# Performance work log

Hardware: AMD Instinct MI355X
Metric: run time of the kernel (lower is better)

Reference implementation:

```python
import jax, jax.numpy as jnp
import numpy as np

N_WORDS = 64
N_CONT_LABELS = 64
N_DISC_LABELS = 32


def _tuple_indices(n):
    # Enumerate (i, k, l, j) with i <= k, l >= k + 2, l <= j < n, matching the
    # nested Python loops in the original forward. Count is static given n.
    ii, kk, ll, jj = np.indices((n, n, n, n), dtype=np.int16)
    mask = (kk >= ii) & (ll >= kk + 2) & (jj >= ll)
    i = ii[mask].astype(np.int32)
    k = kk[mask].astype(np.int32)
    l = ll[mask].astype(np.int32)
    j = jj[mask].astype(np.int32)
    cont_idx = i * n + j                  # row of flattened disc table
    disc_idx = (k + 1) * n + (l - 1)      # row of flattened gap table
    return cont_idx, disc_idx


def setup_inputs() -> dict:
    key = jax.random.key(0)
    n, Lc, Ld = N_WORDS, N_CONT_LABELS, N_DISC_LABELS
    k0, k1, k2, k3, k4 = jax.random.split(key, 5)
    cont_weights = jax.random.normal(k0, (n, n, Lc), dtype=jnp.float32)
    disc_weights = jax.random.normal(k1, (n, n, Ld), dtype=jnp.float32)
    gap_weights = jax.random.normal(k2, (n, n, Ld), dtype=jnp.float32)
    cont_idx_np, disc_idx_np = _tuple_indices(n)  # T = 677040 for n=64
    T = cont_idx_np.shape[0]
    cont_gold = jax.random.randint(k3, (n, n), 0, Lc + 1, dtype=jnp.int32)
    disc_gold = jax.random.randint(k4, (T,), 0, Ld + 1, dtype=jnp.int32)
    return {
        "cont_weights": cont_weights,
        "disc_weights": disc_weights,
        "gap_weights": gap_weights,
        "cont_gold": cont_gold,
        "disc_gold": disc_gold,
        "cont_idx": jnp.asarray(cont_idx_np),
        "disc_idx": jnp.asarray(disc_idx_np),
    }


def reference(cont_weights, disc_weights, gap_weights, cont_gold, disc_gold,
              cont_idx, disc_idx):
    n = cont_weights.shape[0]
    Lc = cont_weights.shape[2]
    Ld = disc_weights.shape[2]
    dt = cont_weights.dtype
    null = jnp.zeros((n, n, 1), dtype=dt)

    # Continuous constituents: per-cell cross-entropy, masked to upper triangle.
    cw = jnp.concatenate([cont_weights, null], axis=-1)          # [n, n, Lc+1]
    log_z = jax.nn.logsumexp(cw, axis=-1)                        # [n, n]
    gold = jnp.take_along_axis(cw, cont_gold[..., None].astype(jnp.int32),
                               axis=-1)[..., 0]                  # [n, n]
    triu = jnp.triu(jnp.ones((n, n), dtype=dt))
    cont_loss = jnp.sum((log_z - gold) * triu)

    # Discontinuous constituents: gather rows of the two tables, add, CE-sum.
    dw = jnp.concatenate([disc_weights, null], axis=-1).reshape(-1, Ld + 1)
    gw = jnp.concatenate([gap_weights, null], axis=-1).reshape(-1, Ld + 1)
    w = dw[cont_idx] + gw[disc_idx]                              # [T, Ld+1]
    gold_d = jnp.take_along_axis(w, disc_gold[:, None].astype(jnp.int32),
                                 axis=1)[:, 0]                   # [T]
    disc_loss = jnp.sum(jax.nn.logsumexp(w, axis=-1) - gold_d)

    return cont_loss + disc_loss
```

## Files before the change

### kernel.cpp

```cpp
#include <hip/hip_runtime.h>

#define N 64
#define LC 64
#define LD 32
#define NCONT (N * N)
#define CONT_BLOCKS 16
#define NPAIRS 1953

typedef __attribute__((ext_vector_type(8))) short short8;
typedef __attribute__((ext_vector_type(4))) float f32x4;

__device__ inline unsigned f2bf(float f) {
    unsigned u = __float_as_uint(f);
    u += 0x7FFF + ((u >> 16) & 1);
    return u >> 16;
}
__device__ inline float bf2f(unsigned u) {
    return __uint_as_float(u << 16);
}

__device__ inline float block_sum(float v, float* ws) {
    #pragma unroll
    for (int off = 32; off > 0; off >>= 1)
        v += __shfl_down(v, off, 64);
    const int lane = threadIdx.x & 63;
    const int wid  = threadIdx.x >> 6;
    if (lane == 0) ws[wid] = v;
    __syncthreads();
    return ws[0] + ws[1] + ws[2] + ws[3];
}

__global__ __launch_bounds__(256, 8) void loss_kernel(
    const float* __restrict__ cont_w,
    const float* __restrict__ disc_w,
    const float* __restrict__ gap_w,
    const int*   __restrict__ cont_gold,
    const int*   __restrict__ disc_gold,
    float* __restrict__ partials, int T)
{
    __shared__ unsigned short EgB[64 * 32];
    __shared__ unsigned short EdB[64 * 32];
    __shared__ float ws[4];

    float acc = 0.0f;

    if (blockIdx.x < CONT_BLOCKS) {
        const int idx = blockIdx.x * 256 + threadIdx.x;
        const int i = idx >> 6, j = idx & 63;
        if (i <= j) {
            const float4* p = reinterpret_cast<const float4*>(cont_w + idx * LC);
            const int g = cont_gold[idx];
            const float goldv = (g < LC) ? cont_w[idx * LC + g] : 0.0f;
            float s0 = 1.0f, s1 = 0.0f, s2 = 0.0f, s3 = 0.0f;
            #pragma unroll
            for (int q = 0; q < LC / 4; ++q) {
                float4 x = p[q];
                s0 += __expf(x.x); s1 += __expf(x.y);
                s2 += __expf(x.z); s3 += __expf(x.w);
            }
            acc = __logf((s0 + s1) + (s2 + s3)) - goldv;
        }
    } else {
        const int w = blockIdx.x - CONT_BLOCKS;
        int k = (int)((sqrtf(8.0f * (float)w + 1.0f) - 1.0f) * 0.5f);
        while (k * (k + 1) / 2 > w) --k;
        while ((k + 1) * (k + 2) / 2 <= w) ++k;
        const int i = w - k * (k + 1) / 2;
        const int M = 62 - k;

        const int MT   = (M + 15) >> 4;
        const int MT16 = MT << 4;
        const float4* srcD = reinterpret_cast<const float4*>(
            disc_w + ((i << 6) + (k + 2)) * LD);
        const float4* srcG = reinterpret_cast<const float4*>(
            gap_w + (((k + 1) << 6) + (k + 1)) * LD);
        for (int e = threadIdx.x; e < MT16 * 8; e += 256) {
            const int r = e >> 3, ch = e & 7;
            uint2* pd = reinterpret_cast<uint2*>(&EdB[r * 32 + ch * 4]);
            uint2* pg = reinterpret_cast<uint2*>(&EgB[r * 32 + ch * 4]);
            if (r < M) {
                float4 x = srcD[e];
                float4 y = srcG[e];
                uint2 xd = { (f2bf(__expf(x.y)) << 16) | f2bf(__expf(x.x)),
                             (f2bf(__expf(x.w)) << 16) | f2bf(__expf(x.z)) };
                uint2 yg = { (f2bf(__expf(y.y)) << 16) | f2bf(__expf(y.x)),
                             (f2bf(__expf(y.w)) << 16) | f2bf(__expf(y.z)) };
                *pd = xd;
                *pg = yg;
            } else {
                uint2 z = {0u, 0u};
                *pd = z;
                *pg = z;
            }
        }
        __syncthreads();

        const int ntiles = MT * (MT + 1) / 2;
        const int wid  = threadIdx.x >> 6;
        const int lane = threadIdx.x & 63;
        const int r16  = lane & 15;
        const int g4   = lane >> 4;
        for (int p = wid; p < ntiles; p += 4) {
            int tr = 0, base = 0;
            while (base + (MT - tr) <= p) { base += MT - tr; ++tr; }
            const int tc = tr + (p - base);
            short8 a = *reinterpret_cast<const short8*>(
                &EgB[(tr * 16 + r16) * 32 + g4 * 8]);
            short8 b = *reinterpret_cast<const short8*>(
                &EdB[(tc * 16 + r16) * 32 + g4 * 8]);
            f32x4 c = {0.0f, 0.0f, 0.0f, 0.0f};
            c = __builtin_amdgcn_mfma_f32_16x16x32_bf16(a, b, c, 0, 0, 0);
            #pragma unroll
            for (int q = 0; q < 4; ++q) {
                const int l = tr * 16 + g4 * 4 + q;
                const int j = tc * 16 + r16;
                if (j < M && l <= j)
                    acc += __logf(c[q] + 1.0f);
            }
        }

        const int A  = 62 - i;
        const int fA = A * (A + 1) * (A + 2) * (A + 3) / 24;
        const int hA = A * (A + 1) * (A + 2) / 6;
        const int hK = M * (M + 1) * (M + 2) / 6;
        const int t0 = (677040 - fA) + (hA - hK);
        const int cells = M * (M + 1) / 2;

        const int Bc = (cells + 255) >> 8;
        const int c0 = threadIdx.x * Bc;
        const int c1 = min(c0 + Bc, cells);
        if (c0 < c1) {
            const float twoM1 = (float)(2 * M + 1);
            int l = (int)((twoM1 - sqrtf(twoM1 * twoM1 - 8.0f * (float)c0)) * 0.5f);
            if (l < 0) l = 0;
            if (l > M - 1) l = M - 1;
            while (l * M - l * (l - 1) / 2 > c0) --l;
            while ((l + 1) * M - (l + 1) * l / 2 <= c0) ++l;
            int j = l + (c0 - (l * M - l * (l - 1) / 2));
            for (int c = c0; c < c1; ++c) {
                const int g = disc_gold[t0 + c];
                if (g < LD) {
                    const float ed = bf2f(EdB[j * 32 + g]);
                    const float eg = bf2f(EgB[l * 32 + g]);
                    acc -= __logf(ed * eg);
                }
                ++j;
                if (j >= M) { ++l; j = l; }
            }
        }
    }

    const float bsum = block_sum(acc, ws);
    if (threadIdx.x == 0)
        partials[blockIdx.x] = bsum;
}

__global__ __launch_bounds__(1024) void reduce_kernel(
    const float* __restrict__ partials, float* __restrict__ out, int nblocks)
{
    float acc = 0.0f;
    for (int i = threadIdx.x; i < nblocks; i += 1024)
        acc += partials[i];
    #pragma unroll
    for (int off = 32; off > 0; off >>= 1)
        acc += __shfl_down(acc, off, 64);

    __shared__ float ws[16];
    const int lane = threadIdx.x & 63;
    const int wid  = threadIdx.x >> 6;
    if (lane == 0) ws[wid] = acc;
    __syncthreads();
    if (threadIdx.x == 0) {
        float s = 0.0f;
        #pragma unroll
        for (int w = 0; w < 16; ++w) s += ws[w];
        out[0] = s;
    }
}

extern "C" void kernel_launch(void* const* d_in, const int* in_sizes, int n_in,
                              void* d_out, int out_size, void* d_ws, size_t ws_size,
                              hipStream_t stream) {
    const float* cont_w    = (const float*)d_in[0];
    const float* disc_w    = (const float*)d_in[1];
    const float* gap_w     = (const float*)d_in[2];
    const int*   cont_gold = (const int*)d_in[3];
    const int*   disc_gold = (const int*)d_in[4];
    float* out      = (float*)d_out;
    float* partials = (float*)d_ws;
    const int T = in_sizes[4];

    const int blocks = CONT_BLOCKS + NPAIRS;
    loss_kernel<<<blocks, 256, 0, stream>>>(cont_w, disc_w, gap_w, cont_gold,
                                            disc_gold, partials, T);
    reduce_kernel<<<1, 1024, 0, stream>>>(partials, out, blocks);
}
```

Before: 14.04 us.

## Pack four work units per 1024-thread block, drop reduce kernel via atomicAdd

Restructures the launch into 256 blocks of 1024 threads, where each block runs four independent 256-thread teams with their own LDS tiles, each team covering two work units in a fixed two-pass loop. The separate reduction kernel is replaced by a memset and a per-block atomicAdd into the output. This is meant to cut the second kernel launch and the block-scheduling overhead of about two thousand small blocks. In exchange, teams now synchronise block-wide, so the slowest team in a block sets the pace. The LDS writes also go from packed 64-bit stores to scalar 16-bit stores, and the atomic summation order is no longer deterministic.

```diff
diff --git a/kernel.cpp b/kernel.cpp
--- a/kernel.cpp
+++ b/kernel.cpp
@@ -3,8 +3,7 @@
 #define N 64
 #define LC 64
 #define LD 32
-#define NCONT (N * N)
-#define CONT_BLOCKS 16
+#define NUNITS 1969
 #define NPAIRS 1953
 
 typedef __attribute__((ext_vector_type(8))) short short8;
@@ -19,162 +18,155 @@
     return __uint_as_float(u << 16);
 }
 
-__device__ inline float block_sum(float v, float* ws) {
-    #pragma unroll
-    for (int off = 32; off > 0; off >>= 1)
-        v += __shfl_down(v, off, 64);
-    const int lane = threadIdx.x & 63;
-    const int wid  = threadIdx.x >> 6;
-    if (lane == 0) ws[wid] = v;
-    __syncthreads();
-    return ws[0] + ws[1] + ws[2] + ws[3];
-}
-
-__global__ __launch_bounds__(256, 8) void loss_kernel(
+__global__ __launch_bounds__(1024, 4) void loss_kernel(
     const float* __restrict__ cont_w,
     const float* __restrict__ disc_w,
     const float* __restrict__ gap_w,
     const int*   __restrict__ cont_gold,
     const int*   __restrict__ disc_gold,
-    float* __restrict__ partials, int T)
+    float* __restrict__ out)
 {
-    __shared__ unsigned short EgB[64 * 32];
-    __shared__ unsigned short EdB[64 * 32];
-    __shared__ float ws[4];
+    __shared__ unsigned short EgB[4][64 * 32];
+    __shared__ unsigned short EdB[4][64 * 32];
+    __shared__ float ws[16];
+
+    const int team  = threadIdx.x >> 8;
+    const int tid   = threadIdx.x & 255;
+    const int gteam = (int)blockIdx.x * 4 + team;
 
     float acc = 0.0f;
 
-    if (blockIdx.x < CONT_BLOCKS) {
-        const int idx = blockIdx.x * 256 + threadIdx.x;
-        const int i = idx >> 6, j = idx & 63;
-        if (i <= j) {
-            const float4* p = reinterpret_cast<const float4*>(cont_w + idx * LC);
-            const int g = cont_gold[idx];
-            const float goldv = (g < LC) ? cont_w[idx * LC + g] : 0.0f;
-            float s0 = 1.0f, s1 = 0.0f, s2 = 0.0f, s3 = 0.0f;
-            #pragma unroll
-            for (int q = 0; q < LC / 4; ++q) {
-                float4 x = p[q];
-                s0 += __expf(x.x); s1 += __expf(x.y);
-                s2 += __expf(x.z); s3 += __expf(x.w);
-            }
-            acc = __logf((s0 + s1) + (s2 + s3)) - goldv;
-        }
-    } else {
-        const int w = blockIdx.x - CONT_BLOCKS;
-        int k = (int)((sqrtf(8.0f * (float)w + 1.0f) - 1.0f) * 0.5f);
-        while (k * (k + 1) / 2 > w) --k;
-        while ((k + 1) * (k + 2) / 2 <= w) ++k;
-        const int i = w - k * (k + 1) / 2;
-        const int M = 62 - k;
+    #pragma unroll
+    for (int rep = 0; rep < 2; ++rep) {
+        const int u = gteam + rep * 1024;
+        const bool valid   = (u < NUNITS);
+        const bool is_cont = valid && (u < 16);
+        const bool is_pair = valid && (u >= 16);
 
-        const int MT   = (M + 15) >> 4;
-        const int MT16 = MT << 4;
-        const float4* srcD = reinterpret_cast<const float4*>(
-            disc_w + ((i << 6) + (k + 2)) * LD);
-        const float4* srcG = reinterpret_cast<const float4*>(
-            gap_w + (((k + 1) << 6) + (k + 1)) * LD);
-        for (int e = threadIdx.x; e < MT16 * 8; e += 256) {
-            const int r = e >> 3, ch = e & 7;
-            uint2* pd = reinterpret_cast<uint2*>(&EdB[r * 32 + ch * 4]);
-            uint2* pg = reinterpret_cast<uint2*>(&EgB[r * 32 + ch * 4]);
-            if (r < M) {
-                float4 x = srcD[e];
-                float4 y = srcG[e];
-                uint2 xd = { (f2bf(__expf(x.y)) << 16) | f2bf(__expf(x.x)),
-                             (f2bf(__expf(x.w)) << 16) | f2bf(__expf(x.z)) };
-                uint2 yg = { (f2bf(__expf(y.y)) << 16) | f2bf(__expf(y.x)),
-                             (f2bf(__expf(y.w)) << 16) | f2bf(__expf(y.z)) };
-                *pd = xd;
-                *pg = yg;
-            } else {
-                uint2 z = {0u, 0u};
-                *pd = z;
-                *pg = z;
+        int i = 0, k = 0, M = 0, MT = 0;
+        if (is_pair) {
+            const int w = u - 16;
+            k = (int)((sqrtf(8.0f * (float)w + 1.0f) - 1.0f) * 0.5f);
+            while (k * (k + 1) / 2 > w) --k;
+            while ((k + 1) * (k + 2) / 2 <= w) ++k;
+            i = w - k * (k + 1) / 2;
+            M = 62 - k;
+            MT = (M + 15) >> 4;
+
+            const int MT16 = MT << 4;
+            const float4* srcD = reinterpret_cast<const float4*>(
+                disc_w + ((i << 6) + (k + 2)) * LD);
+            const float4* srcG = reinterpret_cast<const float4*>(
+                gap_w + (((k + 1) << 6) + (k + 1)) * LD);
+            for (int e = tid; e < MT16 * 8; e += 256) {
+                const int r = e >> 3, ch = e & 7;
+                unsigned short* pd = &EdB[team][r * 32 + ch * 4];
+                unsigned short* pg = &EgB[team][r * 32 + ch * 4];
+                if (r < M) {
+                    float4 x = srcD[e];
+                    float4 y = srcG[e];
+                    pd[0] = (unsigned short)f2bf(__expf(x.x));
+                    pd[1] = (unsigned short)f2bf(__expf(x.y));
+                    pd[2] = (unsigned short)f2bf(__expf(x.z));
+                    pd[3] = (unsigned short)f2bf(__expf(x.w));
+                    pg[0] = (unsigned short)f2bf(__expf(y.x));
+                    pg[1] = (unsigned short)f2bf(__expf(y.y));
+                    pg[2] = (unsigned short)f2bf(__expf(y.z));
+                    pg[3] = (unsigned short)f2bf(__expf(y.w));
+                } else {
+                    pd[0] = 0; pd[1] = 0; pd[2] = 0; pd[3] = 0;
+                    pg[0] = 0; pg[1] = 0; pg[2] = 0; pg[3] = 0;
+                }
             }
         }
         __syncthreads();
 
-        const int ntiles = MT * (MT + 1) / 2;
-        const int wid  = threadIdx.x >> 6;
-        const int lane = threadIdx.x & 63;
-        const int r16  = lane & 15;
-        const int g4   = lane >> 4;
-        for (int p = wid; p < ntiles; p += 4) {
-            int tr = 0, base = 0;
-            while (base + (MT - tr) <= p) { base += MT - tr; ++tr; }
-            const int tc = tr + (p - base);
-            short8 a = *reinterpret_cast<const short8*>(
-                &EgB[(tr * 16 + r16) * 32 + g4 * 8]);
-            short8 b = *reinterpret_cast<const short8*>(
-                &EdB[(tc * 16 + r16) * 32 + g4 * 8]);
-            f32x4 c = {0.0f, 0.0f, 0.0f, 0.0f};
-            c = __builtin_amdgcn_mfma_f32_16x16x32_bf16(a, b, c, 0, 0, 0);
-            #pragma unroll
-            for (int q = 0; q < 4; ++q) {
-                const int l = tr * 16 + g4 * 4 + q;
-                const int j = tc * 16 + r16;
-                if (j < M && l <= j)
-                    acc += __logf(c[q] + 1.0f);
+        if (is_cont) {
+            const int idx = u * 256 + tid;
+            const int ii = idx >> 6, jj = idx & 63;
+            if (ii <= jj) {
+                const float4* p =
+                    reinterpret_cast<const float4*>(cont_w + idx * LC);
+                const int g = cont_gold[idx];
+                const float goldv = (g < LC) ? cont_w[idx * LC + g] : 0.0f;
+                float s0 = 1.0f, s1 = 0.0f, s2 = 0.0f, s3 = 0.0f;
+                #pragma unroll
+                for (int q = 0; q < LC / 4; ++q) {
+                    float4 x = p[q];
+                    s0 += __expf(x.x); s1 += __expf(x.y);
+                    s2 += __expf(x.z); s3 += __expf(x.w);
+                }
+                acc = __logf((s0 + s1) + (s2 + s3)) - goldv;
+            }
+        } else if (is_pair) {
+            const int ntiles = MT * (MT + 1) / 2;
+            const int wid  = tid >> 6;
+            const int lane = tid & 63;
+            const int r16  = lane & 15;
+            const int g4   = lane >> 4;
+            for (int p = wid; p < ntiles; p += 4) {
+                int tr = 0, base = 0;
+                while (base + (MT - tr) <= p) { base += MT - tr; ++tr; }
+                const int tc = tr + (p - base);
+                short8 a = *reinterpret_cast<const short8*>(
+                    &EgB[team][(tr * 16 + r16) * 32 + g4 * 8]);
+                short8 b = *reinterpret_cast<const short8*>(
+                    &EdB[team][(tc * 16 + r16) * 32 + g4 * 8]);
+                f32x4 c = {0.0f, 0.0f, 0.0f, 0.0f};
+                c = __builtin_amdgcn_mfma_f32_16x16x32_bf16(a, b, c, 0, 0, 0);
+                #pragma unroll
+                for (int q = 0; q < 4; ++q) {
+                    const int l = tr * 16 + g4 * 4 + q;
+                    const int j = tc * 16 + r16;
+                    if (j < M && l <= j)
+                        acc += __logf(c[q] + 1.0f);
+                }
+            }
+
+            const int A  = 62 - i;
+            const int fA = A * (A + 1) * (A + 2) * (A + 3) / 24;
+            const int hA = A * (A + 1) * (A + 2) / 6;
+            const int hK = M * (M + 1) * (M + 2) / 6;
+            const int t0 = (677040 - fA) + (hA - hK);
+            const int cells = M * (M + 1) / 2;
+
+            const int Bc = (cells + 255) >> 8;
+            const int c0 = tid * Bc;
+            const int c1 = min(c0 + Bc, cells);
+            if (c0 < c1) {
+                const float twoM1 = (float)(2 * M + 1);
+                int l = (int)((twoM1 -
+                    sqrtf(twoM1 * twoM1 - 8.0f * (float)c0)) * 0.5f);
+                if (l < 0) l = 0;
+                if (l > M - 1) l = M - 1;
+                while (l * M - l * (l - 1) / 2 > c0) --l;
+                while ((l + 1) * M - (l + 1) * l / 2 <= c0) ++l;
+                int j = l + (c0 - (l * M - l * (l - 1) / 2));
+                for (int c = c0; c < c1; ++c) {
+                    const int g = disc_gold[t0 + c];
+                    if (g < LD) {
+                        const float ed = bf2f(EdB[team][j * 32 + g]);
+                        const float eg = bf2f(EgB[team][l * 32 + g]);
+                        acc -= __logf(ed * eg);
+                    }
+                    ++j;
+                    if (j >= M) { ++l; j = l; }
+                }
             }
         }
-
-        const int A  = 62 - i;
-        const int fA = A * (A + 1) * (A + 2) * (A + 3) / 24;
-        const int hA = A * (A + 1) * (A + 2) / 6;
-        const int hK = M * (M + 1) * (M + 2) / 6;
-        const int t0 = (677040 - fA) + (hA - hK);
-        const int cells = M * (M + 1) / 2;
-
-        const int Bc = (cells + 255) >> 8;
-        const int c0 = threadIdx.x * Bc;
-        const int c1 = min(c0 + Bc, cells);
-        if (c0 < c1) {
-            const float twoM1 = (float)(2 * M + 1);
-            int l = (int)((twoM1 - sqrtf(twoM1 * twoM1 - 8.0f * (float)c0)) * 0.5f);
-            if (l < 0) l = 0;
-            if (l > M - 1) l = M - 1;
-            while (l * M - l * (l - 1) / 2 > c0) --l;
-            while ((l + 1) * M - (l + 1) * l / 2 <= c0) ++l;
-            int j = l + (c0 - (l * M - l * (l - 1) / 2));
-            for (int c = c0; c < c1; ++c) {
-                const int g = disc_gold[t0 + c];
-                if (g < LD) {
-                    const float ed = bf2f(EdB[j * 32 + g]);
-                    const float eg = bf2f(EgB[l * 32 + g]);
-                    acc -= __logf(ed * eg);
-                }
-                ++j;
-                if (j >= M) { ++l; j = l; }
-            }
-        }
+        __syncthreads();
     }
 
-    const float bsum = block_sum(acc, ws);
-    if (threadIdx.x == 0)
-        partials[blockIdx.x] = bsum;
-}
-
-__global__ __launch_bounds__(1024) void reduce_kernel(
-    const float* __restrict__ partials, float* __restrict__ out, int nblocks)
-{
-    float acc = 0.0f;
-    for (int i = threadIdx.x; i < nblocks; i += 1024)
-        acc += partials[i];
     #pragma unroll
     for (int off = 32; off > 0; off >>= 1)
         acc += __shfl_down(acc, off, 64);
-
-    __shared__ float ws[16];
-    const int lane = threadIdx.x & 63;
-    const int wid  = threadIdx.x >> 6;
-    if (lane == 0) ws[wid] = acc;
+    if ((threadIdx.x & 63) == 0) ws[threadIdx.x >> 6] = acc;
     __syncthreads();
     if (threadIdx.x == 0) {
         float s = 0.0f;
         #pragma unroll
-        for (int w = 0; w < 16; ++w) s += ws[w];
-        out[0] = s;
+        for (int q = 0; q < 16; ++q) s += ws[q];
+        atomicAdd(out, s);
     }
 }
 
@@ -186,12 +178,9 @@
     const float* gap_w     = (const float*)d_in[2];
     const int*   cont_gold = (const int*)d_in[3];
     const int*   disc_gold = (const int*)d_in[4];
-    float* out      = (float*)d_out;
-    float* partials = (float*)d_ws;
-    const int T = in_sizes[4];
+    float* out = (float*)d_out;
 
-    const int blocks = CONT_BLOCKS + NPAIRS;
-    loss_kernel<<<blocks, 256, 0, stream>>>(cont_w, disc_w, gap_w, cont_gold,
-                                            disc_gold, partials, T);
-    reduce_kernel<<<1, 1024, 0, stream>>>(partials, out, blocks);
+    hipMemsetAsync(out, 0, sizeof(float), stream);
+    loss_kernel<<<256, 1024, 0, stream>>>(cont_w, disc_w, gap_w,
+                                          cont_gold, disc_gold, out);
 }
```

Result: slower. 20.94 us (+49.1%).

## Assign one (i,k) pair per wavefront instead of one per block

Applied to the files above, without the earlier changes.

Each 256-thread block now handles four (i,k) pairs, one per wavefront, with per-wave shared-memory tables, so the __syncthreads barriers and block-level reduction go away. The grid shrinks from about 1969 blocks to 493, and each wave writes its own partial sum. Continuous-cell work is also regrouped per wave. In exchange, each wave handles all MFMA tiles and gold lookups for its pair serially, which lengthens per-wave latency. LDS per block grows fourfold, which may limit occupancy.

```diff
diff --git a/kernel.cpp b/kernel.cpp
--- a/kernel.cpp
+++ b/kernel.cpp
@@ -3,9 +3,9 @@
 #define N 64
 #define LC 64
 #define LD 32
-#define NCONT (N * N)
-#define CONT_BLOCKS 16
 #define NPAIRS 1953
+#define CONT_BLOCKS 4
+#define PAIR_BLOCKS 489
 
 typedef __attribute__((ext_vector_type(8))) short short8;
 typedef __attribute__((ext_vector_type(4))) float f32x4;
@@ -19,147 +19,145 @@
     return __uint_as_float(u << 16);
 }
 
-__device__ inline float block_sum(float v, float* ws) {
-    #pragma unroll
-    for (int off = 32; off > 0; off >>= 1)
-        v += __shfl_down(v, off, 64);
-    const int lane = threadIdx.x & 63;
-    const int wid  = threadIdx.x >> 6;
-    if (lane == 0) ws[wid] = v;
-    __syncthreads();
-    return ws[0] + ws[1] + ws[2] + ws[3];
-}
-
-__global__ __launch_bounds__(256, 8) void loss_kernel(
+__global__ __launch_bounds__(256, 4) void loss_kernel(
     const float* __restrict__ cont_w,
     const float* __restrict__ disc_w,
     const float* __restrict__ gap_w,
     const int*   __restrict__ cont_gold,
     const int*   __restrict__ disc_gold,
-    float* __restrict__ partials, int T)
+    float* __restrict__ partials)
 {
-    __shared__ unsigned short EgB[64 * 32];
-    __shared__ unsigned short EdB[64 * 32];
-    __shared__ float ws[4];
+    __shared__ unsigned short EgB[4][64 * 32];
+    __shared__ unsigned short EdB[4][64 * 32];
+
+    const int wid  = threadIdx.x >> 6;
+    const int lane = threadIdx.x & 63;
 
     float acc = 0.0f;
 
     if (blockIdx.x < CONT_BLOCKS) {
-        const int idx = blockIdx.x * 256 + threadIdx.x;
-        const int i = idx >> 6, j = idx & 63;
-        if (i <= j) {
-            const float4* p = reinterpret_cast<const float4*>(cont_w + idx * LC);
-            const int g = cont_gold[idx];
-            const float goldv = (g < LC) ? cont_w[idx * LC + g] : 0.0f;
-            float s0 = 1.0f, s1 = 0.0f, s2 = 0.0f, s3 = 0.0f;
-            #pragma unroll
-            for (int q = 0; q < LC / 4; ++q) {
-                float4 x = p[q];
-                s0 += __expf(x.x); s1 += __expf(x.y);
-                s2 += __expf(x.z); s3 += __expf(x.w);
+        const int u = blockIdx.x * 4 + wid;
+        #pragma unroll
+        for (int it = 0; it < 4; ++it) {
+            const int idx = u * 256 + it * 64 + lane;
+            const int ii = idx >> 6, jj = idx & 63;
+            if (ii <= jj) {
+                const float4* p =
+                    reinterpret_cast<const float4*>(cont_w + idx * LC);
+                const int g = cont_gold[idx];
+                const float goldv = (g < LC) ? cont_w[idx * LC + g] : 0.0f;
+                float s0 = 1.0f, s1 = 0.0f, s2 = 0.0f, s3 = 0.0f;
+                #pragma unroll
+                for (int q = 0; q < LC / 4; ++q) {
+                    float4 x = p[q];
+                    s0 += __expf(x.x); s1 += __expf(x.y);
+                    s2 += __expf(x.z); s3 += __expf(x.w);
+                }
+                acc += __logf((s0 + s1) + (s2 + s3)) - goldv;
             }
-            acc = __logf((s0 + s1) + (s2 + s3)) - goldv;
         }
     } else {
-        const int w = blockIdx.x - CONT_BLOCKS;
-        int k = (int)((sqrtf(8.0f * (float)w + 1.0f) - 1.0f) * 0.5f);
-        while (k * (k + 1) / 2 > w) --k;
-        while ((k + 1) * (k + 2) / 2 <= w) ++k;
-        const int i = w - k * (k + 1) / 2;
-        const int M = 62 - k;
+        const int w = (blockIdx.x - CONT_BLOCKS) * 4 + wid;
+        if (w < NPAIRS) {
+            int k = (int)((sqrtf(8.0f * (float)w + 1.0f) - 1.0f) * 0.5f);
+            while (k * (k + 1) / 2 > w) --k;
+            while ((k + 1) * (k + 2) / 2 <= w) ++k;
+            const int i = w - k * (k + 1) / 2;
+            const int M = 62 - k;
+            const int MT   = (M + 15) >> 4;
+            const int MT16 = MT << 4;
 
-        const int MT   = (M + 15) >> 4;
-        const int MT16 = MT << 4;
-        const float4* srcD = reinterpret_cast<const float4*>(
-            disc_w + ((i << 6) + (k + 2)) * LD);
-        const float4* srcG = reinterpret_cast<const float4*>(
-            gap_w + (((k + 1) << 6) + (k + 1)) * LD);
-        for (int e = threadIdx.x; e < MT16 * 8; e += 256) {
-            const int r = e >> 3, ch = e & 7;
-            uint2* pd = reinterpret_cast<uint2*>(&EdB[r * 32 + ch * 4]);
-            uint2* pg = reinterpret_cast<uint2*>(&EgB[r * 32 + ch * 4]);
-            if (r < M) {
-                float4 x = srcD[e];
-                float4 y = srcG[e];
-                uint2 xd = { (f2bf(__expf(x.y)) << 16) | f2bf(__expf(x.x)),
-                             (f2bf(__expf(x.w)) << 16) | f2bf(__expf(x.z)) };
-                uint2 yg = { (f2bf(__expf(y.y)) << 16) | f2bf(__expf(y.x)),
-                             (f2bf(__expf(y.w)) << 16) | f2bf(__expf(y.z)) };
-                *pd = xd;
-                *pg = yg;
-            } else {
-                uint2 z = {0u, 0u};
-                *pd = z;
-                *pg = z;
+            const float4* srcD = reinterpret_cast<const float4*>(
+                disc_w + ((i << 6) + (k + 2)) * LD);
+            const float4* srcG = reinterpret_cast<const float4*>(
+                gap_w + (((k + 1) << 6) + (k + 1)) * LD);
+            for (int e = lane; e < MT16 * 8; e += 64) {
+                const int r = e >> 3, ch = e & 7;
+                uint2* pd = reinterpret_cast<uint2*>(&EdB[wid][r * 32 + ch * 4]);
+                uint2* pg = reinterpret_cast<uint2*>(&EgB[wid][r * 32 + ch * 4]);
+                if (r < M) {
+                    float4 x = srcD[e];
+                    float4 y = srcG[e];
+                    uint2 xd = { (f2bf(__expf(x.y)) << 16) | f2bf(__expf(x.x)),
+                                 (f2bf(__expf(x.w)) << 16) | f2bf(__expf(x.z)) };
+                    uint2 yg = { (f2bf(__expf(y.y)) << 16) | f2bf(__expf(y.x)),
+                                 (f2bf(__expf(y.w)) << 16) | f2bf(__expf(y.z)) };
+                    *pd = xd;
+                    *pg = yg;
+                } else {
+                    uint2 z = {0u, 0u};
+                    *pd = z;
+                    *pg = z;
+                }
             }
-        }
-        __syncthreads();
 
-        const int ntiles = MT * (MT + 1) / 2;
-        const int wid  = threadIdx.x >> 6;
-        const int lane = threadIdx.x & 63;
-        const int r16  = lane & 15;
-        const int g4   = lane >> 4;
-        for (int p = wid; p < ntiles; p += 4) {
-            int tr = 0, base = 0;
-            while (base + (MT - tr) <= p) { base += MT - tr; ++tr; }
-            const int tc = tr + (p - base);
-            short8 a = *reinterpret_cast<const short8*>(
-                &EgB[(tr * 16 + r16) * 32 + g4 * 8]);
-            short8 b = *reinterpret_cast<const short8*>(
-                &EdB[(tc * 16 + r16) * 32 + g4 * 8]);
-            f32x4 c = {0.0f, 0.0f, 0.0f, 0.0f};
-            c = __builtin_amdgcn_mfma_f32_16x16x32_bf16(a, b, c, 0, 0, 0);
-            #pragma unroll
-            for (int q = 0; q < 4; ++q) {
-                const int l = tr * 16 + g4 * 4 + q;
-                const int j = tc * 16 + r16;
-                if (j < M && l <= j)
-                    acc += __logf(c[q] + 1.0f);
+            const int ntiles = MT * (MT + 1) / 2;
+            const int r16 = lane & 15;
+            const int g4  = lane >> 4;
+            for (int p = 0; p < ntiles; ++p) {
+                int tr = 0, base = 0;
+                while (base + (MT - tr) <= p) { base += MT - tr; ++tr; }
+                const int tc = tr + (p - base);
+                short8 a = *reinterpret_cast<const short8*>(
+                    &EgB[wid][(tr * 16 + r16) * 32 + g4 * 8]);
+                short8 b = *reinterpret_cast<const short8*>(
+                    &EdB[wid][(tc * 16 + r16) * 32 + g4 * 8]);
+                f32x4 c = {0.0f, 0.0f, 0.0f, 0.0f};
+                c = __builtin_amdgcn_mfma_f32_16x16x32_bf16(a, b, c, 0, 0, 0);
+                #pragma unroll
+                for (int q = 0; q < 4; ++q) {
+                    const int l = tr * 16 + g4 * 4 + q;
+                    const int j = tc * 16 + r16;
+                    if (j < M && l <= j)
+                        acc += __logf(c[q] + 1.0f);
+                }
             }
-        }
 
-        const int A  = 62 - i;
-        const int fA = A * (A + 1) * (A + 2) * (A + 3) / 24;
-        const int hA = A * (A + 1) * (A + 2) / 6;
-        const int hK = M * (M + 1) * (M + 2) / 6;
-        const int t0 = (677040 - fA) + (hA - hK);
-        const int cells = M * (M + 1) / 2;
+            const int A  = 62 - i;
+            const int fA = A * (A + 1) * (A + 2) * (A + 3) / 24;
+            const int hA = A * (A + 1) * (A + 2) / 6;
+            const int hK = M * (M + 1) * (M + 2) / 6;
+            const int t0 = (677040 - fA) + (hA - hK);
+            const int cells = M * (M + 1) / 2;
 
-        const int Bc = (cells + 255) >> 8;
-        const int c0 = threadIdx.x * Bc;
-        const int c1 = min(c0 + Bc, cells);
-        if (c0 < c1) {
-            const float twoM1 = (float)(2 * M + 1);
-            int l = (int)((twoM1 - sqrtf(twoM1 * twoM1 - 8.0f * (float)c0)) * 0.5f);
-            if (l < 0) l = 0;
-            if (l > M - 1) l = M - 1;
-            while (l * M - l * (l - 1) / 2 > c0) --l;
-            while ((l + 1) * M - (l + 1) * l / 2 <= c0) ++l;
-            int j = l + (c0 - (l * M - l * (l - 1) / 2));
-            for (int c = c0; c < c1; ++c) {
-                const int g = disc_gold[t0 + c];
-                if (g < LD) {
-                    const float ed = bf2f(EdB[j * 32 + g]);
-                    const float eg = bf2f(EgB[l * 32 + g]);
-                    acc -= __logf(ed * eg);
+            const int Bc = (cells + 63) >> 6;
+            const int c0 = lane * Bc;
+            const int c1 = min(c0 + Bc, cells);
+            if (c0 < c1) {
+                const float twoM1 = (float)(2 * M + 1);
+                int l = (int)((twoM1 -
+                    sqrtf(twoM1 * twoM1 - 8.0f * (float)c0)) * 0.5f);
+                if (l < 0) l = 0;
+                if (l > M - 1) l = M - 1;
+                while (l * M - l * (l - 1) / 2 > c0) --l;
+                while ((l + 1) * M - (l + 1) * l / 2 <= c0) ++l;
+                int j = l + (c0 - (l * M - l * (l - 1) / 2));
+                for (int c = c0; c < c1; ++c) {
+                    const int g = disc_gold[t0 + c];
+                    if (g < LD) {
+                        const float ed = bf2f(EdB[wid][j * 32 + g]);
+                        const float eg = bf2f(EgB[wid][l * 32 + g]);
+                        acc -= __logf(ed * eg);
+                    }
+                    ++j;
+                    if (j >= M) { ++l; j = l; }
                 }
-                ++j;
-                if (j >= M) { ++l; j = l; }
             }
         }
     }
 
-    const float bsum = block_sum(acc, ws);
-    if (threadIdx.x == 0)
-        partials[blockIdx.x] = bsum;
+    #pragma unroll
+    for (int off = 32; off > 0; off >>= 1)
+        acc += __shfl_down(acc, off, 64);
+    if (lane == 0)
+        partials[blockIdx.x * 4 + wid] = acc;
 }
 
 __global__ __launch_bounds__(1024) void reduce_kernel(
-    const float* __restrict__ partials, float* __restrict__ out, int nblocks)
+    const float* __restrict__ partials, float* __restrict__ out, int nparts)
 {
     float acc = 0.0f;
-    for (int i = threadIdx.x; i < nblocks; i += 1024)
+    for (int i = threadIdx.x; i < nparts; i += 1024)
         acc += partials[i];
     #pragma unroll
     for (int off = 32; off > 0; off >>= 1)
@@ -188,10 +186,9 @@
     const int*   disc_gold = (const int*)d_in[4];
     float* out      = (float*)d_out;
     float* partials = (float*)d_ws;
-    const int T = in_sizes[4];
 
-    const int blocks = CONT_BLOCKS + NPAIRS;
+    const int blocks = CONT_BLOCKS + PAIR_BLOCKS;
     loss_kernel<<<blocks, 256, 0, stream>>>(cont_w, disc_w, gap_w, cont_gold,
-                                            disc_gold, partials, T);
-    reduce_kernel<<<1, 1024, 0, stream>>>(partials, out, blocks);
+                                            disc_gold, partials);
+    reduce_kernel<<<1, 1024, 0, stream>>>(partials, out, blocks * 4);
 }
```

Result: slower. 22.14 us (+57.7%).
